# Performance work log

Measured on AMD Instinct MI355X. Metric: run time of the kernel, lower is better.

The kernel has to match this reference:

```python
import jax, jax.numpy as jnp
import numpy as np
from jax import lax

# Config matching init_kwargs
STRIDE = 1
PAD = 1


def setup_inputs() -> dict:
    key = jax.random.key(0)
    k1, k2, k3, k4 = jax.random.split(key, 4)
    x = jax.random.normal(k1, (8, 64, 128, 128), jnp.float32)
    # offset conv: out_channels = 2*kh*kw = 18, no bias; small init so offsets are moderate
    w_offset = jax.random.normal(k2, (18, 64, 3, 3), jnp.float32) * 0.01
    w_deform = jax.random.normal(k3, (64, 64, 3, 3), jnp.float32) * 0.05
    b_deform = jax.random.normal(k4, (64,), jnp.float32) * 0.05
    return {"x": x, "w_offset": w_offset, "w_deform": w_deform, "b_deform": b_deform}


def _deform_conv2d(x, offset, weight, bias, stride, pad):
    """torchvision.ops.deform_conv2d (v1, offset_groups=1) in pure jax.

    x: [B,C,H,W], offset: [B,2*kh*kw,Ho,Wo] ordered (dy,dx) per kernel tap,
    weight: [O,C,kh,kw], bias: [O].
    """
    B, C, H, W = x.shape
    O, _, kh, kw = weight.shape
    Ho, Wo = offset.shape[2], offset.shape[3]
    K = kh * kw

    off = offset.reshape(B, K, 2, Ho, Wo)  # [...,0]=dy, [...,1]=dx
    ky, kx = jnp.meshgrid(jnp.arange(kh), jnp.arange(kw), indexing="ij")
    base_y = (jnp.arange(Ho) * stride - pad).astype(x.dtype)  # [Ho]
    base_x = (jnp.arange(Wo) * stride - pad).astype(x.dtype)  # [Wo]
    # sampling positions [B,K,Ho,Wo]
    py = base_y[None, None, :, None] + ky.reshape(1, K, 1, 1).astype(x.dtype) + off[:, :, 0]
    px = base_x[None, None, None, :] + kx.reshape(1, K, 1, 1).astype(x.dtype) + off[:, :, 1]

    y0f = jnp.floor(py)
    x0f = jnp.floor(px)
    wy = py - y0f  # bilinear fractional weights [B,K,Ho,Wo]
    wx = px - x0f
    y0 = y0f.astype(jnp.int32)
    x0 = x0f.astype(jnp.int32)

    def gather(yi, xi):
        # zero-padded gather: out-of-bounds samples contribute 0
        valid = (yi >= 0) & (yi < H) & (xi >= 0) & (xi < W)
        yc = jnp.clip(yi, 0, H - 1)
        xc = jnp.clip(xi, 0, W - 1)
        # per-batch fancy gather -> [B, C, K, Ho, Wo]
        g = jax.vmap(lambda im, yy, xx: im[:, yy, xx])(x, yc, xc)
        return g * valid[:, None].astype(x.dtype)

    one = jnp.asarray(1, x.dtype)
    val = (gather(y0, x0) * ((one - wy) * (one - wx))[:, None]
           + gather(y0, x0 + 1) * ((one - wy) * wx)[:, None]
           + gather(y0 + 1, x0) * (wy * (one - wx))[:, None]
           + gather(y0 + 1, x0 + 1) * (wy * wx)[:, None])  # [B,C,K,Ho,Wo]

    out = jnp.einsum("ock,bckij->boij", weight.reshape(O, C, K), val)
    return out + bias[None, :, None, None]


def reference(x, w_offset, w_deform, b_deform):
    # offset-predicting conv (no bias)
    offset = lax.conv_general_dilated(
        x, w_offset, window_strides=(STRIDE, STRIDE),
        padding=[(PAD, PAD), (PAD, PAD)],
        dimension_numbers=("NCHW", "OIHW", "NCHW"))
    return _deform_conv2d(x, offset, w_deform, b_deform, STRIDE, PAD)
```

## Files before the change

### kernel.cpp

```cpp
#include <hip/hip_runtime.h>

#define BATCH 8
#define CIN 64
#define H 128
#define W 128
#define OCH 64
#define HW (H*W)
#define OFFCH 18

using f16x8 = __attribute__((ext_vector_type(8))) _Float16;
using f32x4 = __attribute__((ext_vector_type(4))) float;

static __device__ __forceinline__ int iclamp(int v, int lo, int hi) {
    return v < lo ? lo : (v > hi ? hi : v);
}
static __device__ __forceinline__ f16x8 splat8(_Float16 v) {
    return (f16x8){v, v, v, v, v, v, v, v};
}
static __device__ __forceinline__ unsigned packh2(float a, float b) {
    union { _Float16 h[2]; unsigned u; } pk;
    pk.h[0] = (_Float16)a; pk.h[1] = (_Float16)b;
    return pk.u;
}

__global__ __launch_bounds__(256) void transpose_x_kernel(
    const float* __restrict__ x, _Float16* __restrict__ xt)
{
    __shared__ float ls[CIN][129];
    int bid = blockIdx.x;
    int b = bid >> 7, y = bid & 127;
    int t = threadIdx.x;

    const float* xb = x + (size_t)b * CIN * HW + (size_t)y * W;
    #pragma unroll 4
    for (int i = 0; i < 32; ++i) {
        int c = i * 2 + (t >> 7);
        ls[c][t & 127] = xb[(size_t)c * HW + (t & 127)];
    }
    __syncthreads();

    _Float16* xo = xt + (size_t)(b * H + y) * W * CIN;
    #pragma unroll 4
    for (int i = 0; i < 16; ++i) {
        int px = i * 8 + (t >> 5);
        int c  = (t & 31) * 2;
        _Float16 a0 = (_Float16)ls[c][px];
        _Float16 a1 = (_Float16)ls[c + 1][px];
        union { _Float16 h[2]; unsigned int u; } pk;
        pk.h[0] = a0; pk.h[1] = a1;
        *(unsigned int*)&xo[(size_t)px * CIN + c] = pk.u;
    }
}

__global__ __launch_bounds__(256) void prep_wdf_kernel(
    const float* __restrict__ w, _Float16* __restrict__ wdf)
{
    int i = blockIdx.x * 256 + threadIdx.x;
    if (i >= 9 * 2 * 4 * 64 * 8) return;
    int j    = i & 7;
    int lane = (i >> 3) & 63;
    int mt   = (i >> 9) & 3;
    int cs   = (i >> 11) & 1;
    int tap  = i >> 12;
    int oc = mt * 16 + (lane & 15);
    int c  = cs * 32 + (lane >> 4) * 8 + j;
    wdf[i] = (_Float16)w[(oc * CIN + c) * 9 + tap];
}

__global__ __launch_bounds__(256) void prep_wof_kernel(
    const float* __restrict__ w, _Float16* __restrict__ wof)
{
    int i = blockIdx.x * 256 + threadIdx.x;
    if (i >= 9 * 2 * 2 * 64 * 8) return;
    int j    = i & 7;
    int lane = (i >> 3) & 63;
    int mt   = (i >> 9) & 1;
    int cs   = (i >> 10) & 1;
    int tap  = i >> 11;
    int oc = mt * 16 + (lane & 15);
    int c  = cs * 32 + (lane >> 4) * 8 + j;
    wof[i] = (oc < OFFCH) ? (_Float16)w[(oc * CIN + c) * 9 + tap] : (_Float16)0.f;
}

__global__ __launch_bounds__(1024, 4) void fused_deform_kernel(
    const _Float16* __restrict__ xt, const f16x8* __restrict__ wof,
    const f16x8* __restrict__ wdf, const float* __restrict__ bias,
    float* __restrict__ out)
{
    __shared__ _Float16 band[8 * 128 * CIN];

    int bid  = blockIdx.x;
    int b    = bid & 7;
    int y    = (bid >> 3) * 4;
    int tid  = threadIdx.x;
    int lane = tid & 63;
    int wave = tid >> 6;
    int l15  = lane & 15;
    int lk   = lane >> 4;
    int yo   = y + (wave >> 2);
    int pxbase = (wave & 3) * 32;
    int p0   = pxbase + l15;
    int p1   = p0 + 16;

    int ylo = y - 2 < 0 ? 0 : y - 2;
    int yhi = y + 5 > H - 1 ? H - 1 : y + 5;
    int nrm1 = yhi - ylo;

    const _Float16* xb = xt + (size_t)b * HW * CIN;

    {
        int spx = tid >> 3;
        int sjl = tid & 7;
        int sjp = sjl ^ (spx & 7);
        #pragma unroll
        for (int r = 0; r < 8; ++r) {
            int gy = ylo + r;
            if (gy > yhi) break;
            *(f16x8*)&band[(((size_t)r * 128 + spx) * 8 + sjp) * 8] =
                *(const f16x8*)&xb[((size_t)gy * W + spx) * CIN + sjl * 8];
        }
    }
    __syncthreads();

    f32x4 oacc[2][2];
    #pragma unroll
    for (int mt = 0; mt < 2; ++mt)
        #pragma unroll
        for (int nt = 0; nt < 2; ++nt) oacc[mt][nt] = (f32x4){0.f, 0.f, 0.f, 0.f};

    #pragma unroll
    for (int tap = 0; tap < 9; ++tap) {
        int ky = tap / 3, kx = tap - 3 * ky;
        int yy = yo - 1 + ky;
        bool iny = (yy >= 0 && yy < H);
        int ry = yy - ylo;
        int pos0 = p0 - 1 + kx;
        int pos1 = p1 - 1 + kx;
        #pragma unroll
        for (int cs = 0; cs < 2; ++cs) {
            const f16x8* wf = wof + (size_t)((tap * 2 + cs) * 2) * 64 + lane;
            f16x8 a0 = wf[0];
            f16x8 a1 = wf[64];
            f16x8 b0 = splat8((_Float16)0.f), b1 = splat8((_Float16)0.f);
            if (iny && pos0 >= 0 && pos0 < W) {
                int jp = (cs * 4 + lk) ^ (pos0 & 7);
                b0 = *(const f16x8*)&band[(((size_t)ry * 128 + pos0) * 8 + jp) * 8];
            }
            if (iny && pos1 >= 0 && pos1 < W) {
                int jp = (cs * 4 + lk) ^ (pos1 & 7);
                b1 = *(const f16x8*)&band[(((size_t)ry * 128 + pos1) * 8 + jp) * 8];
            }
            oacc[0][0] = __builtin_amdgcn_mfma_f32_16x16x32_f16(a0, b0, oacc[0][0], 0, 0, 0);
            oacc[1][0] = __builtin_amdgcn_mfma_f32_16x16x32_f16(a1, b0, oacc[1][0], 0, 0, 0);
            oacc[0][1] = __builtin_amdgcn_mfma_f32_16x16x32_f16(a0, b1, oacc[0][1], 0, 0, 0);
            oacc[1][1] = __builtin_amdgcn_mfma_f32_16x16x32_f16(a1, b1, oacc[1][1], 0, 0, 0);
        }
    }

    uint4 rcA, rcB, rcC, rcD;
    uint4 rc8a = {0,0,0,0}, rc8b = {0,0,0,0};
    unsigned ofA, ofB, ofC, ofD, of8a = 0, of8b = 0;

    auto build = [&](int tap, float offy, float offx, int p, uint4& rc, unsigned& of) {
        int ky = tap / 3, kx = tap - 3 * ky;
        float py  = (float)(yo - 1 + ky) + offy;
        float pxf = (float)(p  - 1 + kx) + offx;
        float y0f = floorf(py), x0f = floorf(pxf);
        float fy = py - y0f, fx = pxf - x0f;
        int y0 = (int)y0f, x0 = (int)x0f;
        int y1 = y0 + 1, x1 = x0 + 1;
        float m00 = (1.f - fy) * (1.f - fx);
        float m01 = (1.f - fy) * fx;
        float m10 = fy * (1.f - fx);
        float m11 = fy * fx;
        if (y0 < 0 || y0 >= H) { m00 = 0.f; m01 = 0.f; }
        if (y1 < 0 || y1 >= H) { m10 = 0.f; m11 = 0.f; }
        if (x0 < 0 || x0 >= W) { m00 = 0.f; m10 = 0.f; }
        if (x1 < 0 || x1 >= W) { m01 = 0.f; m11 = 0.f; }
        int y0c = iclamp(y0, 0, H - 1), y1c = iclamp(y1, 0, H - 1);
        int x0c = iclamp(x0, 0, W - 1), x1c = iclamp(x1, 0, W - 1);
        int ry0 = y0c - ylo, ry1 = y1c - ylo;
        unsigned o0 = (ry0 < 0 || ry0 > nrm1) ? 0x8000u : 0u;
        unsigned o1 = (ry1 < 0 || ry1 > nrm1) ? 0x8000u : 0u;
        int r0 = iclamp(ry0, 0, 7), r1 = iclamp(ry1, 0, 7);
        unsigned f0 = (unsigned)(((r0 * 128 + x0c) << 3) | (x0c & 7)) | o0;
        unsigned f1 = (unsigned)(((r0 * 128 + x1c) << 3) | (x1c & 7)) | o0;
        unsigned f2 = (unsigned)(((r1 * 128 + x0c) << 3) | (x0c & 7)) | o1;
        unsigned f3 = (unsigned)(((r1 * 128 + x1c) << 3) | (x1c & 7)) | o1;
        rc.x = packh2(m00, m01);
        rc.y = packh2(m10, m11);
        rc.z = f0 | (f1 << 16);
        rc.w = f2 | (f3 << 16);
        of   = packh2(offy, offx);
    };
    build(2 * lk,     oacc[0][0][0], oacc[0][0][1], p0, rcA, ofA);
    build(2 * lk + 1, oacc[0][0][2], oacc[0][0][3], p0, rcB, ofB);
    build(2 * lk,     oacc[0][1][0], oacc[0][1][1], p1, rcC, ofC);
    build(2 * lk + 1, oacc[0][1][2], oacc[0][1][3], p1, rcD, ofD);
    if (lk == 0) {
        build(8, oacc[1][0][0], oacc[1][0][1], p0, rc8a, of8a);
        build(8, oacc[1][1][0], oacc[1][1][1], p1, rc8b, of8b);
    }

    f32x4 acc[4][2];
    #pragma unroll
    for (int mt = 0; mt < 4; ++mt)
        #pragma unroll
        for (int nt = 0; nt < 2; ++nt) acc[mt][nt] = (f32x4){0.f, 0.f, 0.f, 0.f};

    const char* bb = (const char*)band;

    #pragma unroll
    for (int tap = 0; tap < 9; ++tap) {
        int src = (tap < 8) ? ((tap >> 1) * 16 + l15) : l15;
        f16x8 bfr[2][2];
        #pragma unroll
        for (int nt = 0; nt < 2; ++nt) {
            int pp = nt ? p1 : p0;
            uint4 rsel;
            unsigned osel;
            if (tap < 8) {
                if (tap & 1) { rsel = nt ? rcD : rcB; osel = nt ? ofD : ofB; }
                else         { rsel = nt ? rcC : rcA; osel = nt ? ofC : ofA; }
            } else         { rsel = nt ? rc8b : rc8a; osel = nt ? of8b : of8a; }
            uint4 rc;
            rc.x = (unsigned)__shfl((int)rsel.x, src, 64);
            rc.y = (unsigned)__shfl((int)rsel.y, src, 64);
            rc.z = (unsigned)__shfl((int)rsel.z, src, 64);
            rc.w = (unsigned)__shfl((int)rsel.w, src, 64);

            union { unsigned u; _Float16 h[2]; } mA, mB;
            mA.u = rc.x; mB.u = rc.y;
            _Float16 h00 = mA.h[0], h01 = mA.h[1], h10 = mB.h[0], h11 = mB.h[1];
            int f0 = rc.z & 0xffff, f1 = rc.z >> 16;
            int f2 = rc.w & 0xffff, f3 = rc.w >> 16;
            bool fall = ((rc.z | rc.w) & 0x8000u) != 0;
            int a00 = (((f0 >> 3) & 1023) << 7) + ((lk ^ (f0 & 7)) << 4);
            int a01 = (((f1 >> 3) & 1023) << 7) + ((lk ^ (f1 & 7)) << 4);
            int a10 = (((f2 >> 3) & 1023) << 7) + ((lk ^ (f2 & 7)) << 4);
            int a11 = (((f3 >> 3) & 1023) << 7) + ((lk ^ (f3 & 7)) << 4);

            f16x8 g00 = *(const f16x8*)(bb + a00);
            f16x8 g01 = *(const f16x8*)(bb + a01);
            f16x8 g10 = *(const f16x8*)(bb + a10);
            f16x8 g11 = *(const f16x8*)(bb + a11);
            bfr[0][nt] = g00 * splat8(h00) + g01 * splat8(h01)
                       + g10 * splat8(h10) + g11 * splat8(h11);
            f16x8 k00 = *(const f16x8*)(bb + (a00 ^ 64));
            f16x8 k01 = *(const f16x8*)(bb + (a01 ^ 64));
            f16x8 k10 = *(const f16x8*)(bb + (a10 ^ 64));
            f16x8 k11 = *(const f16x8*)(bb + (a11 ^ 64));
            bfr[1][nt] = k00 * splat8(h00) + k01 * splat8(h01)
                       + k10 * splat8(h10) + k11 * splat8(h11);

            if (__any(fall)) {
                unsigned ofu = (unsigned)__shfl((int)osel, src, 64);
                if (fall) {
                    union { unsigned u; _Float16 h[2]; } of;
                    of.u = ofu;
                    float offy = (float)of.h[0], offx = (float)of.h[1];
                    int ky = tap / 3, kx = tap - 3 * ky;
                    float py  = (float)(yo - 1 + ky) + offy;
                    float pxf = (float)(pp - 1 + kx) + offx;
                    float y0f = floorf(py), x0f = floorf(pxf);
                    float fy = py - y0f, fx = pxf - x0f;
                    int y0 = (int)y0f, x0 = (int)x0f;
                    int y1 = y0 + 1, x1 = x0 + 1;
                    float n00 = (1.f - fy) * (1.f - fx);
                    float n01 = (1.f - fy) * fx;
                    float n10 = fy * (1.f - fx);
                    float n11 = fy * fx;
                    if (y0 < 0 || y0 >= H) { n00 = 0.f; n01 = 0.f; }
                    if (y1 < 0 || y1 >= H) { n10 = 0.f; n11 = 0.f; }
                    if (x0 < 0 || x0 >= W) { n00 = 0.f; n10 = 0.f; }
                    if (x1 < 0 || x1 >= W) { n01 = 0.f; n11 = 0.f; }
                    int y0c = iclamp(y0, 0, H - 1), y1c = iclamp(y1, 0, H - 1);
                    int x0c = iclamp(x0, 0, W - 1), x1c = iclamp(x1, 0, W - 1);
                    _Float16 q00 = (_Float16)n00, q01 = (_Float16)n01;
                    _Float16 q10 = (_Float16)n10, q11 = (_Float16)n11;
                    size_t i00 = ((size_t)y0c * W + x0c) * CIN, i01 = ((size_t)y0c * W + x1c) * CIN;
                    size_t i10 = ((size_t)y1c * W + x0c) * CIN, i11 = ((size_t)y1c * W + x1c) * CIN;
                    int c0 = lk * 8;
                    bfr[0][nt] = (*(const f16x8*)&xb[i00 + c0]) * splat8(q00)
                               + (*(const f16x8*)&xb[i01 + c0]) * splat8(q01)
                               + (*(const f16x8*)&xb[i10 + c0]) * splat8(q10)
                               + (*(const f16x8*)&xb[i11 + c0]) * splat8(q11);
                    int c1 = 32 + lk * 8;
                    bfr[1][nt] = (*(const f16x8*)&xb[i00 + c1]) * splat8(q00)
                               + (*(const f16x8*)&xb[i01 + c1]) * splat8(q01)
                               + (*(const f16x8*)&xb[i10 + c1]) * splat8(q10)
                               + (*(const f16x8*)&xb[i11 + c1]) * splat8(q11);
                }
            }
        }

        #pragma unroll
        for (int cs = 0; cs < 2; ++cs) {
            const f16x8* wf = wdf + (size_t)((tap * 2 + cs) * 4) * 64 + lane;
            #pragma unroll
            for (int mt = 0; mt < 4; ++mt) {
                f16x8 af = wf[mt * 64];
                acc[mt][0] = __builtin_amdgcn_mfma_f32_16x16x32_f16(af, bfr[cs][0], acc[mt][0], 0, 0, 0);
                acc[mt][1] = __builtin_amdgcn_mfma_f32_16x16x32_f16(af, bfr[cs][1], acc[mt][1], 0, 0, 0);
            }
        }
    }

    #pragma unroll
    for (int mt = 0; mt < 4; ++mt) {
        #pragma unroll
        for (int nt = 0; nt < 2; ++nt) {
            int pp = nt ? p1 : p0;
            #pragma unroll
            for (int r = 0; r < 4; ++r) {
                int oc = mt * 16 + lk * 4 + r;
                out[((size_t)b * OCH + oc) * HW + (size_t)yo * W + pp] = acc[mt][nt][r] + bias[oc];
            }
        }
    }
}

extern "C" void kernel_launch(void* const* d_in, const int* in_sizes, int n_in,
                              void* d_out, int out_size, void* d_ws, size_t ws_size,
                              hipStream_t stream) {
    const float* x     = (const float*)d_in[0];
    const float* w_off = (const float*)d_in[1];
    const float* w_def = (const float*)d_in[2];
    const float* b_def = (const float*)d_in[3];
    float* out = (float*)d_out;

    _Float16* xt  = (_Float16*)d_ws;
    _Float16* wdf = xt + (size_t)BATCH * HW * CIN;
    _Float16* wof = wdf + 36864;

    transpose_x_kernel<<<BATCH * H, 256, 0, stream>>>(x, xt);
    prep_wdf_kernel<<<(36864 + 255) / 256, 256, 0, stream>>>(w_def, wdf);
    prep_wof_kernel<<<(18432 + 255) / 256, 256, 0, stream>>>(w_off, wof);
    fused_deform_kernel<<<BATCH * H / 4, 1024, 0, stream>>>(
        xt, (const f16x8*)wof, (const f16x8*)wdf, b_def, out);
}
```

Before: 54.05 us.

## Fuse NCHW-to-NHWC fp16 transpose into deform kernel and merge weight prep kernels

Removes the standalone transpose kernel and its workspace round-trip by having the fused kernel read fp32 NCHW input directly, converting to fp16 while staging the shared-memory band. Fallback bilinear gathers now do per-channel scalar fp32 loads strided by HW instead of vectorized NHWC fp16 loads. The two weight-prep kernels are merged into one launch. This trades a full extra memory pass and launches for less coalesced, more numerous loads in the gather path.

```diff
diff --git a/kernel.cpp b/kernel.cpp
--- a/kernel.cpp
+++ b/kernel.cpp
@@ -23,67 +23,35 @@
     return pk.u;
 }
 
-__global__ __launch_bounds__(256) void transpose_x_kernel(
-    const float* __restrict__ x, _Float16* __restrict__ xt)
-{
-    __shared__ float ls[CIN][129];
-    int bid = blockIdx.x;
-    int b = bid >> 7, y = bid & 127;
-    int t = threadIdx.x;
-
-    const float* xb = x + (size_t)b * CIN * HW + (size_t)y * W;
-    #pragma unroll 4
-    for (int i = 0; i < 32; ++i) {
-        int c = i * 2 + (t >> 7);
-        ls[c][t & 127] = xb[(size_t)c * HW + (t & 127)];
-    }
-    __syncthreads();
-
-    _Float16* xo = xt + (size_t)(b * H + y) * W * CIN;
-    #pragma unroll 4
-    for (int i = 0; i < 16; ++i) {
-        int px = i * 8 + (t >> 5);
-        int c  = (t & 31) * 2;
-        _Float16 a0 = (_Float16)ls[c][px];
-        _Float16 a1 = (_Float16)ls[c + 1][px];
-        union { _Float16 h[2]; unsigned int u; } pk;
-        pk.h[0] = a0; pk.h[1] = a1;
-        *(unsigned int*)&xo[(size_t)px * CIN + c] = pk.u;
-    }
-}
-
-__global__ __launch_bounds__(256) void prep_wdf_kernel(
-    const float* __restrict__ w, _Float16* __restrict__ wdf)
+__global__ __launch_bounds__(256) void prep_w_kernel(
+    const float* __restrict__ wd, const float* __restrict__ wo,
+    _Float16* __restrict__ wdf, _Float16* __restrict__ wof)
 {
     int i = blockIdx.x * 256 + threadIdx.x;
-    if (i >= 9 * 2 * 4 * 64 * 8) return;
-    int j    = i & 7;
-    int lane = (i >> 3) & 63;
-    int mt   = (i >> 9) & 3;
-    int cs   = (i >> 11) & 1;
-    int tap  = i >> 12;
-    int oc = mt * 16 + (lane & 15);
-    int c  = cs * 32 + (lane >> 4) * 8 + j;
-    wdf[i] = (_Float16)w[(oc * CIN + c) * 9 + tap];
-}
-
-__global__ __launch_bounds__(256) void prep_wof_kernel(
-    const float* __restrict__ w, _Float16* __restrict__ wof)
-{
-    int i = blockIdx.x * 256 + threadIdx.x;
-    if (i >= 9 * 2 * 2 * 64 * 8) return;
-    int j    = i & 7;
-    int lane = (i >> 3) & 63;
-    int mt   = (i >> 9) & 1;
-    int cs   = (i >> 10) & 1;
-    int tap  = i >> 11;
-    int oc = mt * 16 + (lane & 15);
-    int c  = cs * 32 + (lane >> 4) * 8 + j;
-    wof[i] = (oc < OFFCH) ? (_Float16)w[(oc * CIN + c) * 9 + tap] : (_Float16)0.f;
+    if (i < 36864) {
+        int j    = i & 7;
+        int lane = (i >> 3) & 63;
+        int mt   = (i >> 9) & 3;
+        int cs   = (i >> 11) & 1;
+        int tap  = i >> 12;
+        int oc = mt * 16 + (lane & 15);
+        int c  = cs * 32 + (lane >> 4) * 8 + j;
+        wdf[i] = (_Float16)wd[(oc * CIN + c) * 9 + tap];
+    } else if (i < 36864 + 18432) {
+        int k = i - 36864;
+        int j    = k & 7;
+        int lane = (k >> 3) & 63;
+        int mt   = (k >> 9) & 1;
+        int cs   = (k >> 10) & 1;
+        int tap  = k >> 11;
+        int oc = mt * 16 + (lane & 15);
+        int c  = cs * 32 + (lane >> 4) * 8 + j;
+        wof[k] = (oc < OFFCH) ? (_Float16)wo[(oc * CIN + c) * 9 + tap] : (_Float16)0.f;
+    }
 }
 
 __global__ __launch_bounds__(1024, 4) void fused_deform_kernel(
-    const _Float16* __restrict__ xt, const f16x8* __restrict__ wof,
+    const float* __restrict__ x, const f16x8* __restrict__ wof,
     const f16x8* __restrict__ wdf, const float* __restrict__ bias,
     float* __restrict__ out)
 {
@@ -106,18 +74,22 @@
     int yhi = y + 5 > H - 1 ? H - 1 : y + 5;
     int nrm1 = yhi - ylo;
 
-    const _Float16* xb = xt + (size_t)b * HW * CIN;
+    const float* xbf = x + (size_t)b * CIN * HW;
 
     {
-        int spx = tid >> 3;
-        int sjl = tid & 7;
-        int sjp = sjl ^ (spx & 7);
+        int px_s = tid & 127;
+        int cg   = tid >> 7;
+        int jp_s = cg ^ (px_s & 7);
+        const float* xcg = xbf + (size_t)(cg * 8) * HW + px_s;
         #pragma unroll
         for (int r = 0; r < 8; ++r) {
             int gy = ylo + r;
             if (gy > yhi) break;
-            *(f16x8*)&band[(((size_t)r * 128 + spx) * 8 + sjp) * 8] =
-                *(const f16x8*)&xb[((size_t)gy * W + spx) * CIN + sjl * 8];
+            const float* xp = xcg + (size_t)gy * W;
+            f16x8 v;
+            #pragma unroll
+            for (int j = 0; j < 8; ++j) v[j] = (_Float16)xp[(size_t)j * HW];
+            *(f16x8*)&band[(((size_t)r * 128 + px_s) * 8 + jp_s) * 8] = v;
         }
     }
     __syncthreads();
@@ -276,20 +248,19 @@
                     if (x1 < 0 || x1 >= W) { n01 = 0.f; n11 = 0.f; }
                     int y0c = iclamp(y0, 0, H - 1), y1c = iclamp(y1, 0, H - 1);
                     int x0c = iclamp(x0, 0, W - 1), x1c = iclamp(x1, 0, W - 1);
-                    _Float16 q00 = (_Float16)n00, q01 = (_Float16)n01;
-                    _Float16 q10 = (_Float16)n10, q11 = (_Float16)n11;
-                    size_t i00 = ((size_t)y0c * W + x0c) * CIN, i01 = ((size_t)y0c * W + x1c) * CIN;
-                    size_t i10 = ((size_t)y1c * W + x0c) * CIN, i11 = ((size_t)y1c * W + x1c) * CIN;
-                    int c0 = lk * 8;
-                    bfr[0][nt] = (*(const f16x8*)&xb[i00 + c0]) * splat8(q00)
-                               + (*(const f16x8*)&xb[i01 + c0]) * splat8(q01)
-                               + (*(const f16x8*)&xb[i10 + c0]) * splat8(q10)
-                               + (*(const f16x8*)&xb[i11 + c0]) * splat8(q11);
-                    int c1 = 32 + lk * 8;
-                    bfr[1][nt] = (*(const f16x8*)&xb[i00 + c1]) * splat8(q00)
-                               + (*(const f16x8*)&xb[i01 + c1]) * splat8(q01)
-                               + (*(const f16x8*)&xb[i10 + c1]) * splat8(q10)
-                               + (*(const f16x8*)&xb[i11 + c1]) * splat8(q11);
+                    int i00 = y0c * W + x0c, i01 = y0c * W + x1c;
+                    int i10 = y1c * W + x0c, i11 = y1c * W + x1c;
+                    #pragma unroll
+                    for (int cs = 0; cs < 2; ++cs) {
+                        const float* xc = xbf + (size_t)(cs * 32 + lk * 8) * HW;
+                        #pragma unroll
+                        for (int j = 0; j < 8; ++j) {
+                            float v = n00 * xc[i00] + n01 * xc[i01]
+                                    + n10 * xc[i10] + n11 * xc[i11];
+                            bfr[cs][nt][j] = (_Float16)v;
+                            xc += HW;
+                        }
+                    }
                 }
             }
         }
@@ -329,13 +300,10 @@
     const float* b_def = (const float*)d_in[3];
     float* out = (float*)d_out;
 
-    _Float16* xt  = (_Float16*)d_ws;
-    _Float16* wdf = xt + (size_t)BATCH * HW * CIN;
+    _Float16* wdf = (_Float16*)d_ws;
     _Float16* wof = wdf + 36864;
 
-    transpose_x_kernel<<<BATCH * H, 256, 0, stream>>>(x, xt);
-    prep_wdf_kernel<<<(36864 + 255) / 256, 256, 0, stream>>>(w_def, wdf);
-    prep_wof_kernel<<<(18432 + 255) / 256, 256, 0, stream>>>(w_off, wof);
+    prep_w_kernel<<<(36864 + 18432 + 255) / 256, 256, 0, stream>>>(w_def, w_off, wdf, wof);
     fused_deform_kernel<<<BATCH * H / 4, 1024, 0, stream>>>(
-        xt, (const f16x8*)wof, (const f16x8*)wdf, b_def, out);
-}
+        x, (const f16x8*)wof, (const f16x8*)wdf, b_def, out);
+}
```

Measured after the change: 47.60 us. 11.9% less time.
